# Optimization experiments

Hardware: AMD Instinct MI355X
Metric: run time of the kernel (lower is better)

## Reference

```python
import jax, jax.numpy as jnp
import numpy as np

B, PHONE_LEN, FRAME_NUM, H = 32, 600, 4096, 256


def setup_inputs() -> dict:
    key = jax.random.key(0)
    ks = jax.random.split(key, 10)
    align = jnp.sort(jax.random.randint(ks[0], (B, FRAME_NUM), 0, 512, dtype=jnp.int64), axis=1)
    return {
        "encoder_out": jax.random.normal(ks[1], (B, PHONE_LEN, H), dtype=jnp.float32),
        "pitch": jax.random.uniform(ks[2], (B, FRAME_NUM), dtype=jnp.float32),
        "beats": jax.random.uniform(ks[3], (B, FRAME_NUM), dtype=jnp.float32),
        "w_pitch": jax.random.normal(ks[4], (H,), dtype=jnp.float32),
        "b_pitch": jax.random.normal(ks[5], (H,), dtype=jnp.float32) * 0.1,
        "w_beats": jax.random.normal(ks[6], (H,), dtype=jnp.float32),
        "b_beats": jax.random.normal(ks[7], (H,), dtype=jnp.float32) * 0.1,
        "w_pos": jax.random.normal(ks[8], (H,), dtype=jnp.float32),
        "b_pos": jax.random.normal(ks[9], (H,), dtype=jnp.float32) * 0.1,
        "align_phone": align,
    }


def _aligner(encoder_out, align_phone):
    # encoder index increments whenever the phone id changes (prev initialized to 0)
    prev = jnp.concatenate(
        [jnp.zeros((align_phone.shape[0], 1), dtype=align_phone.dtype), align_phone[:, :-1]], axis=1
    )
    idx = jnp.cumsum((align_phone != prev).astype(jnp.int32), axis=1)  # [B, T]
    return jnp.take_along_axis(encoder_out, idx[..., None], axis=1)  # [B, T, H]


def reference(encoder_out, pitch, beats, w_pitch, b_pitch, w_beats, b_beats, w_pos, b_pos, align_phone):
    aligned = _aligner(encoder_out, align_phone)                       # [B, T, H]
    T = pitch.shape[1]
    # tiny Linear(1 -> H): scalar * weight + bias, fused additively
    pitch_proj = pitch[..., None] * w_pitch + b_pitch                  # [B, T, H]
    beats_proj = beats[..., None] * w_beats + b_beats                  # [B, T, H]
    pos_scalar = (jnp.arange(T, dtype=aligned.dtype) / T)[:, None]     # [T, 1]
    pos_proj = pos_scalar * w_pos + b_pos                              # [T, H]
    return aligned + pitch_proj + beats_proj + pos_proj
```

## Files before the change

### kernel.cpp

```cpp
#include <hip/hip_runtime.h>

#define B_ 32
#define PHONE_LEN_ 600
#define T_ 4096
#define H_ 256
#define TPB_ 64

typedef float vfloat4 __attribute__((ext_vector_type(4)));

__global__ __launch_bounds__(256) void fuse_kernel(
    const float* __restrict__ enc,
    const float* __restrict__ pitch,
    const float* __restrict__ beats,
    const float* __restrict__ wp, const float* __restrict__ bp,
    const float* __restrict__ wb, const float* __restrict__ bb,
    const float* __restrict__ ws, const float* __restrict__ bs,
    const int* __restrict__ align,
    float* __restrict__ out) {
    const int tid  = threadIdx.x;
    const int lane = tid & 63;
    const int warp = tid >> 6;
    const int b  = blockIdx.y;
    const int t0 = blockIdx.x * TPB_;

    __shared__ unsigned char pres[512];
    __shared__ int pref[512];
    __shared__ int wsum[4];

    const int* __restrict__ arow = align + (size_t)b * T_;

    reinterpret_cast<unsigned short*>(pres)[tid] = 0;
    __syncthreads();
#pragma unroll
    for (int i = 0; i < 16; i += 4) {
        int4 v = *reinterpret_cast<const int4*>(arow + tid * 16 + i);
        pres[v.x] = 1; pres[v.y] = 1; pres[v.z] = 1; pres[v.w] = 1;
    }
    __syncthreads();

    const int p0 = pres[2 * tid];
    const int p1 = pres[2 * tid + 1];
    const int s  = p0 + p1;
    int scan = s;
#pragma unroll
    for (int off = 1; off < 64; off <<= 1) {
        int n = __shfl_up(scan, off, 64);
        if (lane >= off) scan += n;
    }
    if (lane == 63) wsum[warp] = scan;
    __syncthreads();
    int woff = 0;
#pragma unroll
    for (int w = 0; w < 4; ++w) woff += (w < warp) ? wsum[w] : 0;
    const int excl = woff + scan - s;
    pref[2 * tid]     = excl;
    pref[2 * tid + 1] = excl + p0;
    __syncthreads();

    const int adj = (arow[0] != 0) ? 1 : 0;

    const int h4 = lane * 4;
    const float4 w_p = *reinterpret_cast<const float4*>(wp + h4);
    const float4 w_b = *reinterpret_cast<const float4*>(wb + h4);
    const float4 w_s = *reinterpret_cast<const float4*>(ws + h4);
    float4 bsum;
    {
        const float4 b1 = *reinterpret_cast<const float4*>(bp + h4);
        const float4 b2 = *reinterpret_cast<const float4*>(bb + h4);
        const float4 b3 = *reinterpret_cast<const float4*>(bs + h4);
        bsum.x = b1.x + b2.x + b3.x;
        bsum.y = b1.y + b2.y + b3.y;
        bsum.z = b1.z + b2.z + b3.z;
        bsum.w = b1.w + b2.w + b3.w;
    }

    const float invT = 1.0f / (float)T_;
    const int tw = t0 + warp * 16;
#pragma unroll
    for (int tt = 0; tt < 16; ++tt) {
        const int t = tw + tt;
        const size_t bt = (size_t)b * T_ + t;
        const int iv = pref[arow[t]] + adj;
        const float pv = pitch[bt];
        const float bv = beats[bt];
        const float psc = (float)t * invT;

        const float4 e = *reinterpret_cast<const float4*>(
            enc + ((size_t)b * PHONE_LEN_ + iv) * H_ + h4);

        vfloat4 r;
        r.x = e.x + pv * w_p.x + bv * w_b.x + psc * w_s.x + bsum.x;
        r.y = e.y + pv * w_p.y + bv * w_b.y + psc * w_s.y + bsum.y;
        r.z = e.z + pv * w_p.z + bv * w_b.z + psc * w_s.z + bsum.z;
        r.w = e.w + pv * w_p.w + bv * w_b.w + psc * w_s.w + bsum.w;

        __builtin_nontemporal_store(r, reinterpret_cast<vfloat4*>(out + bt * H_ + h4));
    }
}

extern "C" void kernel_launch(void* const* d_in, const int* in_sizes, int n_in,
                              void* d_out, int out_size, void* d_ws, size_t ws_size,
                              hipStream_t stream) {
    const float* enc   = (const float*)d_in[0];
    const float* pitch = (const float*)d_in[1];
    const float* beats = (const float*)d_in[2];
    const float* wp    = (const float*)d_in[3];
    const float* bp    = (const float*)d_in[4];
    const float* wb    = (const float*)d_in[5];
    const float* bb    = (const float*)d_in[6];
    const float* wsp   = (const float*)d_in[7];
    const float* bsp   = (const float*)d_in[8];
    const int*   align = (const int*)d_in[9];

    fuse_kernel<<<dim3(T_ / TPB_, B_), 256, 0, stream>>>(
        enc, pitch, beats, wp, bp, wb, bb, wsp, bsp, align, (float*)d_out);
}
```

Before: 30.63 us.

## Double frames per block and broadcast per-frame scalars via readlane

Each block now covers 128 frames instead of 64, and each warp handles 32 frames, so the per-block presence and prefix-scan setup over the alignment row is spread over twice as much output. The per-frame alignment index, pitch and beats values are loaded once per warp with one coalesced load spread across lanes, then broadcast with readlane. This replaces the scalar per-iteration loads and the dependent LDS lookup inside the loop. The cost is half as many blocks in the grid and a longer unrolled loop that may raise register pressure.

```diff
diff --git a/kernel.cpp b/kernel.cpp
--- a/kernel.cpp
+++ b/kernel.cpp
@@ -4,7 +4,7 @@
 #define PHONE_LEN_ 600
 #define T_ 4096
 #define H_ 256
-#define TPB_ 64
+#define TPB_ 128
 
 typedef float vfloat4 __attribute__((ext_vector_type(4)));
 
@@ -59,6 +59,19 @@
 
     const int adj = (arow[0] != 0) ? 1 : 0;
 
+    const int tw = t0 + warp * 32;
+    const size_t btw = (size_t)b * T_ + tw;
+
+    int   reg_iv;
+    float reg_pb;
+    if (lane < 32) {
+        reg_iv = pref[arow[tw + lane]] + adj;
+        reg_pb = pitch[btw + lane];
+    } else {
+        reg_iv = 0;
+        reg_pb = beats[btw + (lane - 32)];
+    }
+
     const int h4 = lane * 4;
     const float4 w_p = *reinterpret_cast<const float4*>(wp + h4);
     const float4 w_b = *reinterpret_cast<const float4*>(wb + h4);
@@ -75,18 +88,18 @@
     }
 
     const float invT = 1.0f / (float)T_;
-    const int tw = t0 + warp * 16;
+    const float* encb = enc + (size_t)b * PHONE_LEN_ * H_;
+    float* outb = out + (btw)*H_;
+
+    const int ipb = __float_as_int(reg_pb);
 #pragma unroll
-    for (int tt = 0; tt < 16; ++tt) {
-        const int t = tw + tt;
-        const size_t bt = (size_t)b * T_ + t;
-        const int iv = pref[arow[t]] + adj;
-        const float pv = pitch[bt];
-        const float bv = beats[bt];
-        const float psc = (float)t * invT;
+    for (int i = 0; i < 32; ++i) {
+        const int   iv = __builtin_amdgcn_readlane(reg_iv, i);
+        const float pv = __int_as_float(__builtin_amdgcn_readlane(ipb, i));
+        const float bv = __int_as_float(__builtin_amdgcn_readlane(ipb, 32 + i));
+        const float psc = (float)(tw + i) * invT;
 
-        const float4 e = *reinterpret_cast<const float4*>(
-            enc + ((size_t)b * PHONE_LEN_ + iv) * H_ + h4);
+        const float4 e = *reinterpret_cast<const float4*>(encb + iv * H_ + h4);
 
         vfloat4 r;
         r.x = e.x + pv * w_p.x + bv * w_b.x + psc * w_s.x + bsum.x;
@@ -94,7 +107,7 @@
         r.z = e.z + pv * w_p.z + bv * w_b.z + psc * w_s.z + bsum.z;
         r.w = e.w + pv * w_p.w + bv * w_b.w + psc * w_s.w + bsum.w;
 
-        __builtin_nontemporal_store(r, reinterpret_cast<vfloat4*>(out + bt * H_ + h4));
+        __builtin_nontemporal_store(r, reinterpret_cast<vfloat4*>(outb + i * H_ + h4));
     }
 }
 
```

Result: faster. 28.25 us (median of 2 runs) (-7.8%).
